# Kernel optimization log

Measured on AMD Instinct MI355X. Metric: run time of the kernel, lower is better.

The kernel has to match this reference:

```python
import jax, jax.numpy as jnp
import numpy as np
from jax import lax

B, S, D_MODEL, H, P = 16, 2048, 512, 8, 128
DEPTH = D_MODEL // H          # 64
C = (S + P - 1) // P          # chunk_size = 16


def _build_table():
    # table[R-1, c, :] = indices of positions assigned to cluster c when R real tokens,
    # padded with R (the padded zero-row index when R == S, else first pad position).
    table = np.zeros((S, P, C), dtype=np.int32)
    cols = np.arange(C)
    for R in range(1, S + 1):
        assign = np.minimum(np.arange(R) * P // R, P - 1)  # nondecreasing
        starts = np.searchsorted(assign, np.arange(P), side='left')
        ends = np.searchsorted(assign, np.arange(P), side='right')
        cand = starts[:, None] + cols[None, :]
        table[R - 1] = np.where(cand < ends[:, None], cand, R)
    return table


def setup_inputs() -> dict:
    key = jax.random.key(0)
    ks = jax.random.split(key, 12)
    def glorot(k, shp):
        fan = shp[-2] + shp[-1]
        return jax.random.normal(k, shp, jnp.float32) * np.sqrt(2.0 / fan).astype(np.float32)
    x = jax.random.normal(ks[0], (B, S, D_MODEL), jnp.float32)
    lengths = jax.random.randint(ks[1], (B,), S // 2, S + 1)
    mask = jnp.arange(S)[None, :] < lengths[:, None]
    return dict(
        x=x, mask=mask,
        wq=glorot(ks[2], (D_MODEL, D_MODEL)),
        wk=glorot(ks[3], (D_MODEL, D_MODEL)),
        wv=glorot(ks[4], (D_MODEL, D_MODEL)),
        e_w=glorot(ks[5], (H, P, C)),
        f_w=glorot(ks[6], (H, P, C)),
        ck1=glorot(ks[7], (1, P, 1, 1)), cb1=jnp.zeros((1,), jnp.float32),
        ck3=glorot(ks[8], (3, P, 1, 1)), cb3=jnp.zeros((1,), jnp.float32),
        ck5=glorot(ks[9], (5, P, 1, 1)), cb5=jnp.zeros((1,), jnp.float32),
        dw=glorot(ks[10], (D_MODEL, D_MODEL)),
        db=jnp.zeros((D_MODEL,), jnp.float32),
        table=jnp.asarray(_build_table()),
    )


def _conv_same(z, kern, bias):
    # z: (N, S, P, 1), kern: (h, P, 1, 1); Keras Conv2D padding='same', stride 1
    return lax.conv_general_dilated(
        z, kern, window_strides=(1, 1), padding='SAME',
        dimension_numbers=('NHWC', 'HWIO', 'NHWC')) + bias


def _forward(x, mask, wq, wk, wv, e_w, f_w, ck1, cb1, ck3, cb3, ck5, cb5, dw, db, table):
    b = x.shape[0]
    split = lambda t: t.reshape(b, S, H, DEPTH).transpose(0, 2, 1, 3)  # (B,H,S,depth)
    q = split(x @ wq)
    k = split(x @ wk)
    v = split(x @ wv)
    pad = ((0, 0), (0, 0), (0, 1), (0, 0))
    k = jnp.pad(k, pad)  # (B,H,S+1,depth) zero pad row at index S
    v = jnp.pad(v, pad)
    real_counts = jnp.clip(jnp.sum(mask.astype(jnp.int32), axis=1), 1, S)
    pos = table[real_counts - 1]                  # (B,P,C) per-batch cluster index table
    gather = jax.vmap(lambda t, idx: t[:, idx])   # gather over seq axis per batch
    k_ch = gather(k, pos)                          # (B,H,P,C,depth)
    v_ch = gather(v, pos)
    k_proj = jnp.einsum('bhpcd,hpc->bhpd', k_ch, e_w)
    v_proj = jnp.einsum('bhpcd,hpc->bhpd', v_ch, f_w)
    scores = jnp.einsum('bhsd,bhpd->bhsp', q, k_proj) / jnp.sqrt(jnp.float32(DEPTH))
    z = scores.reshape(b * H, S, P, 1)
    # mean of the three conv branches (filter heights 1,3,5)
    conv_avg = (_conv_same(z, ck1, cb1) + _conv_same(z, ck3, cb3) + _conv_same(z, ck5, cb5)) / 3.0
    scores = conv_avg.reshape(b, H, S, P)
    w = jax.nn.softmax(scores, axis=-1)
    attn = jnp.einsum('bhsp,bhpd->bhsd', w, v_proj)
    concat = attn.transpose(0, 2, 1, 3).reshape(b, S, D_MODEL)
    return concat @ dw + db


def reference(x, mask, wq, wk, wv, e_w, f_w, ck1, cb1, ck3, cb3, ck5, cb5, dw, db, table):
    return _forward(x, mask, wq, wk, wv, e_w, f_w, ck1, cb1, ck3, cb3, ck5, cb5, dw, db, table)
```

## Files before the change

### kernel.cpp

```cpp
#include <hip/hip_runtime.h>
#include <hip/hip_bf16.h>

#define BN 16
#define SN 2048
#define DM 512
#define HN 8
#define PN 128
#define DEPTH 64
#define CSZ 16

typedef unsigned short u16;
typedef __bf16 bf16x8 __attribute__((ext_vector_type(8)));
typedef float f32x4 __attribute__((ext_vector_type(4)));

#define OFF_QB   0ull
#define OFF_KB   8388608ull
#define OFF_VB   16777216ull
#define OFF_CB   25165824ull
#define OFF_WQT  33554432ull
#define OFF_WKT  33685504ull
#define OFF_WVT  33816576ull
#define OFF_DWT  33947648ull
#define OFF_KP   34078720ull
#define OFF_VPT  35127296ull
#define OFF_KEP  35651584ull
#define OFF_EFF  38273024ull
#define OFF_CNT  38273664ull
#define OFF_XB   38273792ull

__device__ __forceinline__ u16 f2bf(float f) {
    unsigned u = __float_as_uint(f);
    u = (u + 0x7fffu + ((u >> 16) & 1u)) >> 16;
    return (u16)u;
}
__device__ __forceinline__ float b2f(u16 h) {
    return __uint_as_float(((unsigned)h) << 16);
}

__device__ __forceinline__ void xcd_decode(int bid, int nmem, int& g, int& j) {
    int xcd = bid & 7;
    int t = bid >> 3;
    j = t % nmem;
    g = (t / nmem) * 8 + xcd;
}

__global__ void count_kernel(const void* mask, int* counts) {
    __shared__ int red[256];
    int b = blockIdx.x, tid = threadIdx.x;
    const unsigned char* mb = (const unsigned char*)mask;
    bool is_byte = (mb[1] != 0);
    int local = 0;
    if (is_byte) {
        const unsigned char* row = mb + (size_t)b * SN;
        for (int s = tid; s < SN; s += 256) local += (row[s] != 0);
    } else {
        const int* row = (const int*)mask + (size_t)b * SN;
        for (int s = tid; s < SN; s += 256) local += (row[s] != 0);
    }
    red[tid] = local;
    __syncthreads();
    for (int st = 128; st > 0; st >>= 1) {
        if (tid < st) red[tid] += red[tid + st];
        __syncthreads();
    }
    if (tid == 0) {
        int c = red[0];
        if (c < 1) c = 1;
        if (c > SN) c = SN;
        counts[b] = c;
    }
}

__global__ void eff_kernel(const float* ck1, const float* ck3, const float* ck5, float* eff) {
    int i = threadIdx.x;
    if (i < 640) {
        int t = i >> 7, j = i & 127;
        float v = ck5[t * 128 + j];
        if (t >= 1 && t <= 3) v += ck3[(t - 1) * 128 + j];
        if (t == 2) v += ck1[j];
        eff[i] = v * (1.0f / 3.0f);
    }
}

__global__ __launch_bounds__(256) void convert_x_kernel(const float* __restrict__ x, u16* __restrict__ xb) {
    size_t i = ((size_t)blockIdx.x * 256 + threadIdx.x) * 16;
#pragma unroll
    for (int k = 0; k < 4; k++) {
        float4 v = *(const float4*)&x[i + k * 4];
        ushort4 o;
        o.x = f2bf(v.x); o.y = f2bf(v.y); o.z = f2bf(v.z); o.w = f2bf(v.w);
        *(ushort4*)&xb[i + k * 4] = o;
    }
}

__global__ void convert_wT_kernel(const float* w0, const float* w1, const float* w2, const float* w3,
                                  u16* o0, u16* o1, u16* o2, u16* o3) {
    int z = blockIdx.z;
    const float* W = (z == 0) ? w0 : (z == 1) ? w1 : (z == 2) ? w2 : w3;
    u16* O = (z == 0) ? o0 : (z == 1) ? o1 : (z == 2) ? o2 : o3;
    __shared__ float t[32][33];
    int k0 = blockIdx.y * 32, n0 = blockIdx.x * 32;
    int lx = threadIdx.x & 31, ly = threadIdx.x >> 5;
#pragma unroll
    for (int i = 0; i < 4; i++) t[ly + i * 8][lx] = W[(size_t)(k0 + ly + i * 8) * 512 + n0 + lx];
    __syncthreads();
#pragma unroll
    for (int i = 0; i < 4; i++) O[(size_t)(n0 + ly + i * 8) * 512 + k0 + lx] = f2bf(t[lx][ly + i * 8]);
}

__global__ __launch_bounds__(256) void gemm_qkv(const u16* __restrict__ A,
                                                const u16* __restrict__ WT,
                                                u16* __restrict__ Q,
                                                u16* __restrict__ K,
                                                u16* __restrict__ V) {
    __shared__ __align__(16) char smem[32768];
    char* AsB = smem;
    char* BsB = smem + 16384;

    int g, mem;
    xcd_decode(blockIdx.x, 12, g, mem);
    const int z = mem >> 2;
    const int m0 = g * 128, n0 = (mem & 3) * 128;
    const int tid = threadIdx.x;
    const int w = tid >> 6, l = tid & 63;
    const int wm = w >> 1, wn = w & 1;
    const int lr = l >> 3, sp = l & 7;
    const int slog = sp ^ lr;
    const int cl = l & 15, kg = l >> 4;

    const char* Ab = (const char*)A;
    const char* Bb = (const char*)(WT + (size_t)z * 262144);

    f32x4 acc[4][4];
    const f32x4 z4 = {0.f, 0.f, 0.f, 0.f};
#pragma unroll
    for (int mf = 0; mf < 4; mf++)
#pragma unroll
        for (int nf = 0; nf < 4; nf++) acc[mf][nf] = z4;

    for (int kt = 0; kt < 8; kt++) {
        __syncthreads();
#pragma unroll
        for (int i = 0; i < 4; i++) {
            int c = w * 4 + i;
            const char* ga = Ab + (size_t)(m0 + c * 8 + lr) * 1024 + kt * 128 + slog * 16;
            __builtin_amdgcn_global_load_lds((const __attribute__((address_space(1))) void*)ga,
                                             (__attribute__((address_space(3))) void*)(AsB + c * 1024),
                                             16, 0, 0);
            const char* gb = Bb + (size_t)(n0 + c * 8 + lr) * 1024 + kt * 128 + slog * 16;
            __builtin_amdgcn_global_load_lds((const __attribute__((address_space(1))) void*)gb,
                                             (__attribute__((address_space(3))) void*)(BsB + c * 1024),
                                             16, 0, 0);
        }
        __syncthreads();
#pragma unroll
        for (int ks = 0; ks < 2; ks++) {
            bf16x8 a[4], b[4];
#pragma unroll
            for (int mf = 0; mf < 4; mf++) {
                int row = wm * 64 + mf * 16 + cl;
                a[mf] = *(const bf16x8*)(AsB + row * 128 + (((ks * 4 + kg) ^ (row & 7)) * 16));
            }
#pragma unroll
            for (int nf = 0; nf < 4; nf++) {
                int row = wn * 64 + nf * 16 + cl;
                b[nf] = *(const bf16x8*)(BsB + row * 128 + (((ks * 4 + kg) ^ (row & 7)) * 16));
            }
#pragma unroll
            for (int mf = 0; mf < 4; mf++)
#pragma unroll
                for (int nf = 0; nf < 4; nf++)
                    acc[mf][nf] = __builtin_amdgcn_mfma_f32_16x16x32_bf16(a[mf], b[nf], acc[mf][nf], 0, 0, 0);
        }
    }

    const int rl = l >> 4;
    u16* Ob = (z == 0) ? Q : (z == 1) ? K : V;
#pragma unroll
    for (int mf = 0; mf < 4; mf++)
#pragma unroll
        for (int nf = 0; nf < 4; nf++) {
            f32x4 v = acc[mf][nf];
            int n = n0 + wn * 64 + nf * 16 + cl;
            int h = n >> 6, d = n & 63;
#pragma unroll
            for (int r = 0; r < 4; r++) {
                int m = m0 + wm * 64 + mf * 16 + rl * 4 + r;
                int b = m >> 11, s = m & 2047;
                Ob[(size_t)((b * HN + h) * SN + s) * DEPTH + d] = f2bf(v[r]);
            }
        }
}

__global__ __launch_bounds__(256) void gemm_out(const u16* __restrict__ A,
                                                const u16* __restrict__ WT,
                                                float* __restrict__ O,
                                                const float* __restrict__ bias) {
    __shared__ __align__(16) char smem[32768];
    char* AsB = smem;
    char* BsB = smem + 16384;

    int g, j;
    xcd_decode(blockIdx.x, 4, g, j);
    const int m0 = g * 128, n0 = j * 128;
    const int tid = threadIdx.x;
    const int w = tid >> 6, l = tid & 63;
    const int wm = w >> 1, wn = w & 1;
    const int lr = l >> 3, sp = l & 7;
    const int slog = sp ^ lr;
    const int cl = l & 15, kg = l >> 4;

    const char* Ab = (const char*)A;
    const char* Bb = (const char*)WT;

    f32x4 acc[4][4];
    const f32x4 z4 = {0.f, 0.f, 0.f, 0.f};
#pragma unroll
    for (int mf = 0; mf < 4; mf++)
#pragma unroll
        for (int nf = 0; nf < 4; nf++) acc[mf][nf] = z4;

    for (int kt = 0; kt < 8; kt++) {
        __syncthreads();
#pragma unroll
        for (int i = 0; i < 4; i++) {
            int c = w * 4 + i;
            const char* ga = Ab + (size_t)(m0 + c * 8 + lr) * 1024 + kt * 128 + slog * 16;
            __builtin_amdgcn_global_load_lds((const __attribute__((address_space(1))) void*)ga,
                                             (__attribute__((address_space(3))) void*)(AsB + c * 1024),
                                             16, 0, 0);
            const char* gb = Bb + (size_t)(n0 + c * 8 + lr) * 1024 + kt * 128 + slog * 16;
            __builtin_amdgcn_global_load_lds((const __attribute__((address_space(1))) void*)gb,
                                             (__attribute__((address_space(3))) void*)(BsB + c * 1024),
                                             16, 0, 0);
        }
        __syncthreads();
#pragma unroll
        for (int ks = 0; ks < 2; ks++) {
            bf16x8 a[4], b[4];
#pragma unroll
            for (int mf = 0; mf < 4; mf++) {
                int row = wm * 64 + mf * 16 + cl;
                a[mf] = *(const bf16x8*)(AsB + row * 128 + (((ks * 4 + kg) ^ (row & 7)) * 16));
            }
#pragma unroll
            for (int nf = 0; nf < 4; nf++) {
                int row = wn * 64 + nf * 16 + cl;
                b[nf] = *(const bf16x8*)(BsB + row * 128 + (((ks * 4 + kg) ^ (row & 7)) * 16));
            }
#pragma unroll
            for (int mf = 0; mf < 4; mf++)
#pragma unroll
                for (int nf = 0; nf < 4; nf++)
                    acc[mf][nf] = __builtin_amdgcn_mfma_f32_16x16x32_bf16(a[mf], b[nf], acc[mf][nf], 0, 0, 0);
        }
    }

    const int rl = l >> 4;
#pragma unroll
    for (int mf = 0; mf < 4; mf++)
#pragma unroll
        for (int nf = 0; nf < 4; nf++) {
            f32x4 v = acc[mf][nf];
            int n = n0 + wn * 64 + nf * 16 + cl;
            float bs = bias[n];
#pragma unroll
            for (int r = 0; r < 4; r++) {
                int m = m0 + wm * 64 + mf * 16 + rl * 4 + r;
                O[(size_t)m * 512 + n] = v[r] + bs;
            }
        }
}

__global__ void kvproj_kernel(const u16* __restrict__ Kin, const u16* __restrict__ Vin,
                              const int* __restrict__ table, const int* __restrict__ counts,
                              const float* __restrict__ e_w, const float* __restrict__ f_w,
                              float* __restrict__ kproj, u16* __restrict__ vpT) {
    int p = blockIdx.x;
    int b = blockIdx.y;
    int tid = threadIdx.x;
    int h = tid >> 6, d = tid & 63;
    __shared__ int poss[16];
    __shared__ float ew_s[8][16], fw_s[8][16];
    if (tid < 16) {
        int R = counts[b];
        poss[tid] = table[(size_t)(R - 1) * PN * CSZ + p * CSZ + tid];
    } else if (tid >= 64 && tid < 192) {
        int t2 = tid - 64;
        ew_s[t2 >> 4][t2 & 15] = e_w[(size_t)((t2 >> 4) * PN + p) * CSZ + (t2 & 15)];
    } else if (tid >= 192 && tid < 320) {
        int t2 = tid - 192;
        fw_s[t2 >> 4][t2 & 15] = f_w[(size_t)((t2 >> 4) * PN + p) * CSZ + (t2 & 15)];
    }
    __syncthreads();
    float ka = 0.f, va = 0.f;
    size_t base = (size_t)(b * HN + h) * SN * DEPTH + d;
#pragma unroll
    for (int c = 0; c < CSZ; c++) {
        int idx = poss[c];
        if (idx < SN) {
            float kv = b2f(Kin[base + (size_t)idx * DEPTH]);
            float vv = b2f(Vin[base + (size_t)idx * DEPTH]);
            ka = fmaf(ew_s[h][c], kv, ka);
            va = fmaf(fw_s[h][c], vv, va);
        }
    }
    int bh = b * HN + h;
    kproj[((size_t)bh * PN + p) * DEPTH + d] = ka;
    vpT[(size_t)bh * 8192 + d * 128 + p] = f2bf(va);
}

__global__ __launch_bounds__(256) void ke_kernel(const float* __restrict__ kproj,
                                                 const float* __restrict__ eff,
                                                 u16* __restrict__ keP) {
    int blk = blockIdx.x;
    int bh = blk >> 1;
    int dh = (blk & 1) * 32;
    int tid = threadIdx.x;
    int p = tid & 127;
    int sub = (tid >> 7) * 16;

    __shared__ float kpad[256 * 48];
    __shared__ float ef[640];

    for (int i = tid; i < 256 * 48; i += 256) kpad[i] = 0.f;
    for (int i = tid; i < 640; i += 256) ef[i] = eff[i];
    __syncthreads();
    for (int i = tid; i < 128 * 8; i += 256) {
        int row = i >> 3, c4 = (i & 7) * 4;
        float4 v = *(const float4*)&kproj[(size_t)bh * 8192 + row * 64 + dh + c4];
        *(float4*)&kpad[(64 + row) * 48 + c4] = v;
    }
    __syncthreads();

    float4 acc[5][4];
#pragma unroll
    for (int t = 0; t < 5; t++)
#pragma unroll
        for (int i = 0; i < 4; i++) acc[t][i] = make_float4(0.f, 0.f, 0.f, 0.f);

    for (int j = 0; j < 128; j++) {
        int rr = p + j + 1;
        float4 kv[4];
#pragma unroll
        for (int i = 0; i < 4; i++) kv[i] = *(const float4*)&kpad[rr * 48 + sub + i * 4];
        float w[5];
#pragma unroll
        for (int t = 0; t < 5; t++) w[t] = ef[t * 128 + j];
#pragma unroll
        for (int t = 0; t < 5; t++)
#pragma unroll
            for (int i = 0; i < 4; i++) {
                acc[t][i].x = fmaf(w[t], kv[i].x, acc[t][i].x);
                acc[t][i].y = fmaf(w[t], kv[i].y, acc[t][i].y);
                acc[t][i].z = fmaf(w[t], kv[i].z, acc[t][i].z);
                acc[t][i].w = fmaf(w[t], kv[i].w, acc[t][i].w);
            }
    }

    size_t obase = (size_t)bh * 40960 + (size_t)p * 320;
#pragma unroll
    for (int t = 0; t < 5; t++)
#pragma unroll
        for (int i = 0; i < 4; i++) {
            int d0 = dh + sub + i * 4;
            ushort4 o;
            o.x = f2bf(acc[t][i].x * 0.125f);
            o.y = f2bf(acc[t][i].y * 0.125f);
            o.z = f2bf(acc[t][i].z * 0.125f);
            o.w = f2bf(acc[t][i].w * 0.125f);
            *(ushort4*)&keP[obase + t * 64 + d0] = o;
        }
}

__global__ __launch_bounds__(256) void attn_kernel(const u16* __restrict__ qg,
                                                   const u16* __restrict__ keP,
                                                   const u16* __restrict__ vpT,
                                                   u16* __restrict__ concat) {
    __shared__ __align__(16) char smem[32768];
    char* qswz = smem;
    char* keB = smem + 8704;
    char* wlds = smem;
    char* vps = smem + 16384;

    int bh, st;
    xcd_decode(blockIdx.x, 32, bh, st);
    const int b = bh >> 3, h = bh & 7;
    const int s0 = st * 64;
    const int tid = threadIdx.x;
    const int w = tid >> 6, l = tid & 63;
    const int cl = l & 15, kg = l >> 4;

    const u16* qb = qg + (size_t)bh * SN * DEPTH;
    for (int i = tid; i < 68 * 8; i += 256) {
        int row = i >> 3, slot = i & 7;
        int srow = s0 + row - 2;
        int4 val = make_int4(0, 0, 0, 0);
        if (srow >= 0 && srow < SN)
            val = *(const int4*)(qb + (size_t)srow * 64 + slot * 8);
        *(int4*)(qswz + row * 128 + ((slot ^ (row & 7)) * 16)) = val;
    }

    f32x4 acc[8];
    const f32x4 z4 = {0.f, 0.f, 0.f, 0.f};
#pragma unroll
    for (int nf = 0; nf < 8; nf++) acc[nf] = z4;

    const char* kePb = (const char*)(keP + (size_t)bh * 40960);
    for (int kt = 0; kt < 5; kt++) {
        __syncthreads();
#pragma unroll
        for (int it = 0; it < 4; it++) {
            int i = it * 256 + tid;
            int p = i >> 3, slot = i & 7;
            const char* src = kePb + 2 * ((size_t)p * 320 + kt * 64) + ((slot ^ (p & 7)) * 16);
            __builtin_amdgcn_global_load_lds((const __attribute__((address_space(1))) void*)src,
                                             (__attribute__((address_space(3))) void*)(keB + i * 16),
                                             16, 0, 0);
        }
        __syncthreads();
#pragma unroll
        for (int ks = 0; ks < 2; ks++) {
            int slot = ks * 4 + kg;
            int arow = w * 16 + kt + cl;
            bf16x8 af = *(const bf16x8*)(qswz + arow * 128 + ((slot ^ (arow & 7)) * 16));
#pragma unroll
            for (int nf = 0; nf < 8; nf++) {
                int prow = nf * 16 + cl;
                bf16x8 bf = *(const bf16x8*)(keB + prow * 128 + ((slot ^ (prow & 7)) * 16));
                acc[nf] = __builtin_amdgcn_mfma_f32_16x16x32_bf16(af, bf, acc[nf], 0, 0, 0);
            }
        }
    }
    __syncthreads();

    const char* vpb = (const char*)(vpT + (size_t)bh * 8192);
#pragma unroll
    for (int it = 0; it < 4; it++) {
        int i = it * 256 + tid;
        int d = i >> 4, slot = i & 15;
        const char* src = vpb + 2 * ((size_t)d * 128) + ((slot ^ (d & 7)) * 16);
        __builtin_amdgcn_global_load_lds((const __attribute__((address_space(1))) void*)src,
                                         (__attribute__((address_space(3))) void*)(vps + i * 16),
                                         16, 0, 0);
    }

    float inv[4];
#pragma unroll
    for (int r = 0; r < 4; r++) {
        float m = acc[0][r];
#pragma unroll
        for (int nf = 1; nf < 8; nf++) m = fmaxf(m, acc[nf][r]);
        m = fmaxf(m, __shfl_xor(m, 1));
        m = fmaxf(m, __shfl_xor(m, 2));
        m = fmaxf(m, __shfl_xor(m, 4));
        m = fmaxf(m, __shfl_xor(m, 8));
        float s = 0.f;
#pragma unroll
        for (int nf = 0; nf < 8; nf++) {
            float e = __expf(acc[nf][r] - m);
            acc[nf][r] = e;
            s += e;
        }
        s += __shfl_xor(s, 1);
        s += __shfl_xor(s, 2);
        s += __shfl_xor(s, 4);
        s += __shfl_xor(s, 8);
        inv[r] = 1.0f / s;
    }
#pragma unroll
    for (int r = 0; r < 4; r++) {
        int row = w * 16 + kg * 4 + r;
#pragma unroll
        for (int nf = 0; nf < 8; nf++) {
            int col = nf * 16 + cl;
            int slot = col >> 3, within = col & 7;
            *(u16*)(wlds + row * 256 + ((slot ^ (row & 7)) * 8 + within) * 2) = f2bf(acc[nf][r] * inv[r]);
        }
    }
    __syncthreads();

    f32x4 acc2[4];
#pragma unroll
    for (int nf = 0; nf < 4; nf++) acc2[nf] = z4;
#pragma unroll
    for (int ks = 0; ks < 4; ks++) {
        int slot = ks * 4 + kg;
        int arow = w * 16 + cl;
        bf16x8 af = *(const bf16x8*)(wlds + arow * 256 + ((slot ^ (arow & 7)) * 16));
#pragma unroll
        for (int nf = 0; nf < 4; nf++) {
            int drow = nf * 16 + cl;
            bf16x8 bf = *(const bf16x8*)(vps + drow * 256 + ((slot ^ (drow & 7)) * 16));
            acc2[nf] = __builtin_amdgcn_mfma_f32_16x16x32_bf16(af, bf, acc2[nf], 0, 0, 0);
        }
    }
#pragma unroll
    for (int nf = 0; nf < 4; nf++) {
#pragma unroll
        for (int r = 0; r < 4; r++) {
            int srow = s0 + w * 16 + kg * 4 + r;
            int d = nf * 16 + cl;
            concat[((size_t)b * SN + srow) * DM + h * 64 + d] = f2bf(acc2[nf][r]);
        }
    }
}

extern "C" void kernel_launch(void* const* d_in, const int* in_sizes, int n_in,
                              void* d_out, int out_size, void* d_ws, size_t ws_size,
                              hipStream_t stream) {
    const float* x = (const float*)d_in[0];
    const void* mask = d_in[1];
    const float* wq = (const float*)d_in[2];
    const float* wk = (const float*)d_in[3];
    const float* wv = (const float*)d_in[4];
    const float* e_w = (const float*)d_in[5];
    const float* f_w = (const float*)d_in[6];
    const float* ck1 = (const float*)d_in[7];
    const float* ck3 = (const float*)d_in[9];
    const float* ck5 = (const float*)d_in[11];
    const float* dw = (const float*)d_in[13];
    const float* db = (const float*)d_in[14];
    const int* table = (const int*)d_in[15];

    float* ws = (float*)d_ws;
    u16* qb = (u16*)(ws + OFF_QB);
    u16* kb = (u16*)(ws + OFF_KB);
    u16* vb = (u16*)(ws + OFF_VB);
    u16* cb = (u16*)(ws + OFF_CB);
    u16* xb = (u16*)(ws + OFF_XB);
    u16* wqT = (u16*)(ws + OFF_WQT);
    u16* wkT = (u16*)(ws + OFF_WKT);
    u16* wvT = (u16*)(ws + OFF_WVT);
    u16* dwT = (u16*)(ws + OFF_DWT);
    float* kp = ws + OFF_KP;
    u16* vpT = (u16*)(ws + OFF_VPT);
    u16* keP = (u16*)(ws + OFF_KEP);
    float* eff = ws + OFF_EFF;
    int* counts = (int*)(ws + OFF_CNT);
    float* out = (float*)d_out;

    count_kernel<<<dim3(16), dim3(256), 0, stream>>>(mask, counts);
    eff_kernel<<<dim3(1), dim3(640), 0, stream>>>(ck1, ck3, ck5, eff);
    convert_x_kernel<<<dim3(4096), dim3(256), 0, stream>>>(x, xb);
    convert_wT_kernel<<<dim3(16, 16, 4), dim3(256), 0, stream>>>(wq, wk, wv, dw, wqT, wkT, wvT, dwT);
    gemm_qkv<<<dim3(3072), dim3(256), 0, stream>>>(xb, wqT, qb, kb, vb);
    kvproj_kernel<<<dim3(128, 16), dim3(512), 0, stream>>>(kb, vb, table, counts, e_w, f_w, kp, vpT);
    ke_kernel<<<dim3(256), dim3(256), 0, stream>>>(kp, eff, keP);
    attn_kernel<<<dim3(4096), dim3(256), 0, stream>>>(qb, keP, vpT, cb);
    gemm_out<<<dim3(1024), dim3(256), 0, stream>>>(cb, dwT, out, db);
}
```

Measured before the change: 227.9 us.

## Reassociate K/V projection: gather-and-weight x first, then project clusters

Instead of computing full K and V projections over all 2048 positions and then gathering and weighting per cluster, x is gathered and weighted with e_w/f_w per head first (producing a 128-row matrix per head and batch). A small GEMM against the per-head slice of Wk/Wv then yields k_proj and v_proj directly. This removes two thirds of the large QKV GEMM and its K/V writes, in exchange for a new gather kernel that writes a 16x larger intermediate G and an extra GEMM launch. Rounding changes because weighted sums of x are stored in bf16 before projection.

```diff
diff --git a/kernel.cpp b/kernel.cpp
--- a/kernel.cpp
+++ b/kernel.cpp
@@ -14,8 +14,7 @@
 typedef float f32x4 __attribute__((ext_vector_type(4)));
 
 #define OFF_QB   0ull
-#define OFF_KB   8388608ull
-#define OFF_VB   16777216ull
+#define OFF_G    8388608ull
 #define OFF_CB   25165824ull
 #define OFF_WQT  33554432ull
 #define OFF_WKT  33685504ull
@@ -108,19 +107,16 @@
     for (int i = 0; i < 4; i++) O[(size_t)(n0 + ly + i * 8) * 512 + k0 + lx] = f2bf(t[lx][ly + i * 8]);
 }
 
-__global__ __launch_bounds__(256) void gemm_qkv(const u16* __restrict__ A,
-                                                const u16* __restrict__ WT,
-                                                u16* __restrict__ Q,
-                                                u16* __restrict__ K,
-                                                u16* __restrict__ V) {
+__global__ __launch_bounds__(256) void gemm_q(const u16* __restrict__ A,
+                                              const u16* __restrict__ WT,
+                                              u16* __restrict__ Q) {
     __shared__ __align__(16) char smem[32768];
     char* AsB = smem;
     char* BsB = smem + 16384;
 
-    int g, mem;
-    xcd_decode(blockIdx.x, 12, g, mem);
-    const int z = mem >> 2;
-    const int m0 = g * 128, n0 = (mem & 3) * 128;
+    int g, j;
+    xcd_decode(blockIdx.x, 4, g, j);
+    const int m0 = g * 128, n0 = j * 128;
     const int tid = threadIdx.x;
     const int w = tid >> 6, l = tid & 63;
     const int wm = w >> 1, wn = w & 1;
@@ -129,7 +125,7 @@
     const int cl = l & 15, kg = l >> 4;
 
     const char* Ab = (const char*)A;
-    const char* Bb = (const char*)(WT + (size_t)z * 262144);
+    const char* Bb = (const char*)WT;
 
     f32x4 acc[4][4];
     const f32x4 z4 = {0.f, 0.f, 0.f, 0.f};
@@ -175,7 +171,6 @@
     }
 
     const int rl = l >> 4;
-    u16* Ob = (z == 0) ? Q : (z == 1) ? K : V;
 #pragma unroll
     for (int mf = 0; mf < 4; mf++)
 #pragma unroll
@@ -187,7 +182,7 @@
             for (int r = 0; r < 4; r++) {
                 int m = m0 + wm * 64 + mf * 16 + rl * 4 + r;
                 int b = m >> 11, s = m & 2047;
-                Ob[(size_t)((b * HN + h) * SN + s) * DEPTH + d] = f2bf(v[r]);
+                Q[(size_t)((b * HN + h) * SN + s) * DEPTH + d] = f2bf(v[r]);
             }
         }
 }
@@ -272,42 +267,136 @@
         }
 }
 
-__global__ void kvproj_kernel(const u16* __restrict__ Kin, const u16* __restrict__ Vin,
-                              const int* __restrict__ table, const int* __restrict__ counts,
-                              const float* __restrict__ e_w, const float* __restrict__ f_w,
-                              float* __restrict__ kproj, u16* __restrict__ vpT) {
+__global__ __launch_bounds__(256) void gather_kernel(const u16* __restrict__ xb,
+                                                     const int* __restrict__ table, const int* __restrict__ counts,
+                                                     const float* __restrict__ e_w, const float* __restrict__ f_w,
+                                                     u16* __restrict__ G) {
     int p = blockIdx.x;
     int b = blockIdx.y;
     int tid = threadIdx.x;
-    int h = tid >> 6, d = tid & 63;
     __shared__ int poss[16];
     __shared__ float ew_s[8][16], fw_s[8][16];
     if (tid < 16) {
         int R = counts[b];
         poss[tid] = table[(size_t)(R - 1) * PN * CSZ + p * CSZ + tid];
-    } else if (tid >= 64 && tid < 192) {
-        int t2 = tid - 64;
-        ew_s[t2 >> 4][t2 & 15] = e_w[(size_t)((t2 >> 4) * PN + p) * CSZ + (t2 & 15)];
-    } else if (tid >= 192 && tid < 320) {
-        int t2 = tid - 192;
-        fw_s[t2 >> 4][t2 & 15] = f_w[(size_t)((t2 >> 4) * PN + p) * CSZ + (t2 & 15)];
+    }
+    {
+        int t2 = tid & 127;
+        int h = t2 >> 4, c = t2 & 15;
+        float v = ((tid < 128) ? e_w : f_w)[(size_t)(h * PN + p) * CSZ + c];
+        if (tid < 128) ew_s[h][c] = v; else fw_s[h][c] = v;
     }
     __syncthreads();
-    float ka = 0.f, va = 0.f;
-    size_t base = (size_t)(b * HN + h) * SN * DEPTH + d;
-#pragma unroll
-    for (int c = 0; c < CSZ; c++) {
-        int idx = poss[c];
-        if (idx < SN) {
-            float kv = b2f(Kin[base + (size_t)idx * DEPTH]);
-            float vv = b2f(Vin[base + (size_t)idx * DEPTH]);
-            ka = fmaf(ew_s[h][c], kv, ka);
-            va = fmaf(fw_s[h][c], vv, va);
-        }
-    }
-    int bh = b * HN + h;
-    kproj[((size_t)bh * PN + p) * DEPTH + d] = ka;
-    vpT[(size_t)bh * 8192 + d * 128 + p] = f2bf(va);
+
+    const u16* xrow = xb + (size_t)b * SN * 512;
+#pragma unroll
+    for (int half = 0; half < 2; half++) {
+        int dm = half * 256 + tid;
+        float ak[8] = {0.f, 0.f, 0.f, 0.f, 0.f, 0.f, 0.f, 0.f};
+        float av[8] = {0.f, 0.f, 0.f, 0.f, 0.f, 0.f, 0.f, 0.f};
+#pragma unroll
+        for (int c = 0; c < 16; c++) {
+            int pos = poss[c];
+            if (pos < SN) {
+                float xv = b2f(xrow[(size_t)pos * 512 + dm]);
+#pragma unroll
+                for (int h = 0; h < 8; h++) {
+                    ak[h] = fmaf(ew_s[h][c], xv, ak[h]);
+                    av[h] = fmaf(fw_s[h][c], xv, av[h]);
+                }
+            }
+        }
+#pragma unroll
+        for (int h = 0; h < 8; h++) {
+            G[((size_t)(h * 16 + b) * 128 + p) * 512 + dm] = f2bf(ak[h]);
+            G[((size_t)((8 + h) * 16 + b) * 128 + p) * 512 + dm] = f2bf(av[h]);
+        }
+    }
+}
+
+__global__ __launch_bounds__(256) void proj_kernel(const u16* __restrict__ G,
+                                                   const u16* __restrict__ wkT, const u16* __restrict__ wvT,
+                                                   float* __restrict__ kp, u16* __restrict__ vpT) {
+    __shared__ __align__(16) char smem[24576];
+    char* AsB = smem;
+    char* BsB = smem + 16384;
+
+    const int mt = blockIdx.x;
+    const int kv = mt >> 7, h = (mt >> 4) & 7, bb = mt & 15;
+    const int tid = threadIdx.x;
+    const int w = tid >> 6, l = tid & 63;
+    const int wm = w >> 1, wn = w & 1;
+    const int lr = l >> 3, sp = l & 7;
+    const int slog = sp ^ lr;
+    const int cl = l & 15, kg = l >> 4;
+
+    const char* Ab = (const char*)(G + (size_t)mt * 65536);
+    const char* Bb = (const char*)((kv ? wvT : wkT) + (size_t)h * 64 * 512);
+
+    f32x4 acc[4][2];
+    const f32x4 z4 = {0.f, 0.f, 0.f, 0.f};
+#pragma unroll
+    for (int mf = 0; mf < 4; mf++)
+#pragma unroll
+        for (int nf = 0; nf < 2; nf++) acc[mf][nf] = z4;
+
+    for (int kt = 0; kt < 8; kt++) {
+        __syncthreads();
+#pragma unroll
+        for (int i = 0; i < 4; i++) {
+            int c = w * 4 + i;
+            const char* ga = Ab + (size_t)(c * 8 + lr) * 1024 + kt * 128 + slog * 16;
+            __builtin_amdgcn_global_load_lds((const __attribute__((address_space(1))) void*)ga,
+                                             (__attribute__((address_space(3))) void*)(AsB + c * 1024),
+                                             16, 0, 0);
+        }
+#pragma unroll
+        for (int i = 0; i < 2; i++) {
+            int c = w * 2 + i;
+            const char* gb = Bb + (size_t)(c * 8 + lr) * 1024 + kt * 128 + slog * 16;
+            __builtin_amdgcn_global_load_lds((const __attribute__((address_space(1))) void*)gb,
+                                             (__attribute__((address_space(3))) void*)(BsB + c * 1024),
+                                             16, 0, 0);
+        }
+        __syncthreads();
+#pragma unroll
+        for (int ks = 0; ks < 2; ks++) {
+            bf16x8 a[4], b[2];
+#pragma unroll
+            for (int mf = 0; mf < 4; mf++) {
+                int row = wm * 64 + mf * 16 + cl;
+                a[mf] = *(const bf16x8*)(AsB + row * 128 + (((ks * 4 + kg) ^ (row & 7)) * 16));
+            }
+#pragma unroll
+            for (int nf = 0; nf < 2; nf++) {
+                int row = wn * 32 + nf * 16 + cl;
+                b[nf] = *(const bf16x8*)(BsB + row * 128 + (((ks * 4 + kg) ^ (row & 7)) * 16));
+            }
+#pragma unroll
+            for (int mf = 0; mf < 4; mf++)
+#pragma unroll
+                for (int nf = 0; nf < 2; nf++)
+                    acc[mf][nf] = __builtin_amdgcn_mfma_f32_16x16x32_bf16(a[mf], b[nf], acc[mf][nf], 0, 0, 0);
+        }
+    }
+
+    const int rl = l >> 4;
+    const int bh = bb * HN + h;
+#pragma unroll
+    for (int mf = 0; mf < 4; mf++)
+#pragma unroll
+        for (int nf = 0; nf < 2; nf++) {
+            f32x4 v = acc[mf][nf];
+            int d = wn * 32 + nf * 16 + cl;
+#pragma unroll
+            for (int r = 0; r < 4; r++) {
+                int p = wm * 64 + mf * 16 + rl * 4 + r;
+                if (kv == 0)
+                    kp[((size_t)bh * PN + p) * DEPTH + d] = v[r];
+                else
+                    vpT[(size_t)bh * 8192 + d * 128 + p] = f2bf(v[r]);
+            }
+        }
 }
 
 __global__ __launch_bounds__(256) void ke_kernel(const float* __restrict__ kproj,
@@ -525,8 +614,7 @@
 
     float* ws = (float*)d_ws;
     u16* qb = (u16*)(ws + OFF_QB);
-    u16* kb = (u16*)(ws + OFF_KB);
-    u16* vb = (u16*)(ws + OFF_VB);
+    u16* G = (u16*)(ws + OFF_G);
     u16* cb = (u16*)(ws + OFF_CB);
     u16* xb = (u16*)(ws + OFF_XB);
     u16* wqT = (u16*)(ws + OFF_WQT);
@@ -544,8 +632,9 @@
     eff_kernel<<<dim3(1), dim3(640), 0, stream>>>(ck1, ck3, ck5, eff);
     convert_x_kernel<<<dim3(4096), dim3(256), 0, stream>>>(x, xb);
     convert_wT_kernel<<<dim3(16, 16, 4), dim3(256), 0, stream>>>(wq, wk, wv, dw, wqT, wkT, wvT, dwT);
-    gemm_qkv<<<dim3(3072), dim3(256), 0, stream>>>(xb, wqT, qb, kb, vb);
-    kvproj_kernel<<<dim3(128, 16), dim3(512), 0, stream>>>(kb, vb, table, counts, e_w, f_w, kp, vpT);
+    gemm_q<<<dim3(1024), dim3(256), 0, stream>>>(xb, wqT, qb);
+    gather_kernel<<<dim3(128, 16), dim3(256), 0, stream>>>(xb, table, counts, e_w, f_w, G);
+    proj_kernel<<<dim3(256), dim3(256), 0, stream>>>(G, wkT, wvT, kp, vpT);
     ke_kernel<<<dim3(256), dim3(256), 0, stream>>>(kp, eff, keP);
     attn_kernel<<<dim3(4096), dim3(256), 0, stream>>>(qb, keP, vpT, cb);
     gemm_out<<<dim3(1024), dim3(256), 0, stream>>>(cb, dwT, out, db);
```

After: 214.3 us. 6.0% less time.
